# Kernel optimization log

Measured on AMD Instinct MI355X. Metric: run time of the kernel, lower is better.

The kernel has to match this reference:

```python
import jax, jax.numpy as jnp
import numpy as np

B, H, W, C_TOT = 8, 256, 256, 36
SIDX = slice(0, 3)    # special: Noll 1-3 -> 0-based 0..2
LIDX = slice(3, 6)    # low
MIDX = slice(6, 15)   # mid
HIDX = slice(15, 36)  # high


def _box3x3_sum(x):
    # x: [B, H, W]; 3x3 sliding-window sum with replicate (edge) padding.
    xp = jnp.pad(x, ((0, 0), (1, 1), (1, 1)), mode='edge')
    h, w = x.shape[1], x.shape[2]
    acc = jnp.zeros_like(x)
    for di in range(3):
        for dj in range(3):
            acc = acc + xp[:, di:di + h, dj:dj + w]
    return acc


def _group_core(z, bias, alpha, amax, eps, gss, p_sat):
    # z: [B, H, W, Cg]; all params shape [1]
    u = z + bias
    soft_abs = jnp.sqrt(u * u + eps)            # [B,H,W,Cg]
    s = _box3x3_sum(soft_abs.sum(axis=-1))      # [B,H,W] sum over channels and 3x3 window
    gain = gss / (1.0 + s / p_sat)              # [B,H,W]
    v = alpha * gain[..., None] * u
    return amax * jnp.tanh(v)


def setup_inputs() -> dict:
    key = jax.random.key(0)
    one = jnp.ones((1,), jnp.float32)
    inp = {
        'raw_coeffs': jax.random.normal(key, (B, H, W, C_TOT), dtype=jnp.float32),
        'special_bias': 0.0 * one, 'special_alpha': 1.0 * one,
        'special_amax': 1.0 * one, 'special_eps': 1e-6 * one,
        'low_bias': 0.0 * one, 'low_alpha': 1.0 * one, 'low_amax': 1.0 * one,
        'low_eps': 1e-6 * one, 'low_gss': 1.0 * one, 'low_p_sat': 1.0 * one,
        'mid_bias': 0.0 * one, 'mid_alpha': 1.0 * one, 'mid_amax': 1.0 * one,
        'mid_eps': 1e-6 * one, 'mid_gss': 1.0 * one, 'mid_p_sat': 1.0 * one,
        'high_bias': 0.0 * one, 'high_alpha': 1.0 * one, 'high_amax': 1.0 * one,
        'high_eps': 1e-6 * one, 'high_gss': 1.0 * one, 'high_p_sat': 1.0 * one,
    }
    return inp


def reference(raw_coeffs, special_bias, special_alpha, special_amax, special_eps,
              low_bias, low_alpha, low_amax, low_eps, low_gss, low_p_sat,
              mid_bias, mid_alpha, mid_amax, mid_eps, mid_gss, mid_p_sat,
              high_bias, high_alpha, high_amax, high_eps, high_gss, high_p_sat):
    # special group: plain affine + tanh (special_use_neighborhood=False)
    u_sp = raw_coeffs[..., SIDX] + special_bias
    out_sp = special_amax * jnp.tanh(special_alpha * u_sp)
    # local joint (3x3 coupled gain) groups
    out_lo = _group_core(raw_coeffs[..., LIDX], low_bias, low_alpha, low_amax, low_eps, low_gss, low_p_sat)
    out_mi = _group_core(raw_coeffs[..., MIDX], mid_bias, mid_alpha, mid_amax, mid_eps, mid_gss, mid_p_sat)
    out_hi = _group_core(raw_coeffs[..., HIDX], high_bias, high_alpha, high_amax, high_eps, high_gss, high_p_sat)
    return jnp.concatenate([out_sp, out_lo, out_mi, out_hi], axis=-1)
```

## Files before the change

kernel.cpp:

```cpp
#include <hip/hip_runtime.h>
#include <math.h>


static constexpr int IMG = 256;
static constexpr int NB = 8;
static constexpr int C = 36;
static constexpr int TS = 16;
static constexpr int HT = TS + 2;
static constexpr int ROWF4 = HT * 9;
static constexpr int NSTAGE4 = HT * HT * 9;
static constexpr int NOUT4 = TS * TS * 9;

__device__ __forceinline__ float fast_tanh(float x) {
    float e = __expf(2.0f * x);
    return 1.0f - __fdividef(2.0f, e + 1.0f);
}

__device__ __forceinline__ void group_sums(const float* __restrict__ v,
                                           float b_lo, float e_lo,
                                           float b_mi, float e_mi,
                                           float b_hi, float e_hi,
                                           float& tlo, float& tmi, float& thi) {
    float lo = 0.f, mi = 0.f, hi = 0.f;
    #pragma unroll
    for (int c = 3; c < 6; ++c)   { float u = v[c] + b_lo; lo += sqrtf(u * u + e_lo); }
    #pragma unroll
    for (int c = 6; c < 15; ++c)  { float u = v[c] + b_mi; mi += sqrtf(u * u + e_mi); }
    #pragma unroll
    for (int c = 15; c < 36; ++c) { float u = v[c] + b_hi; hi += sqrtf(u * u + e_hi); }
    tlo = lo; tmi = mi; thi = hi;
}

__global__ __launch_bounds__(256) void lgz_kernel(
    const float* __restrict__ in, float* __restrict__ out,
    const float* __restrict__ p_sp_bias, const float* __restrict__ p_sp_alpha,
    const float* __restrict__ p_sp_amax,
    const float* __restrict__ p_lo_bias, const float* __restrict__ p_lo_alpha,
    const float* __restrict__ p_lo_amax, const float* __restrict__ p_lo_eps,
    const float* __restrict__ p_lo_gss, const float* __restrict__ p_lo_psat,
    const float* __restrict__ p_mi_bias, const float* __restrict__ p_mi_alpha,
    const float* __restrict__ p_mi_amax, const float* __restrict__ p_mi_eps,
    const float* __restrict__ p_mi_gss, const float* __restrict__ p_mi_psat,
    const float* __restrict__ p_hi_bias, const float* __restrict__ p_hi_alpha,
    const float* __restrict__ p_hi_amax, const float* __restrict__ p_hi_eps,
    const float* __restrict__ p_hi_gss, const float* __restrict__ p_hi_psat)
{
    __shared__ __align__(16) float s_raw[HT * HT * C];
    __shared__ float s_sum[3][HT][HT + 1];

    const int tid = threadIdx.x;
    const int tx = tid & 15, ty = tid >> 4;
    const int bx0 = blockIdx.x * TS, by0 = blockIdx.y * TS;
    const int b = blockIdx.z;

    const float b_sp = p_sp_bias[0], a_sp = p_sp_alpha[0], m_sp = p_sp_amax[0];
    const float b_lo = p_lo_bias[0], a_lo = p_lo_alpha[0], m_lo = p_lo_amax[0];
    const float e_lo = p_lo_eps[0],  g_lo = p_lo_gss[0],  q_lo = p_lo_psat[0];
    const float b_mi = p_mi_bias[0], a_mi = p_mi_alpha[0], m_mi = p_mi_amax[0];
    const float e_mi = p_mi_eps[0],  g_mi = p_mi_gss[0],  q_mi = p_mi_psat[0];
    const float b_hi = p_hi_bias[0], a_hi = p_hi_alpha[0], m_hi = p_hi_amax[0];
    const float e_hi = p_hi_eps[0],  g_hi = p_hi_gss[0],  q_hi = p_hi_psat[0];

    const float* img = in + (size_t)b * IMG * IMG * C;
    float* outimg = out + (size_t)b * IMG * IMG * C;

    #pragma unroll
    for (int it = 0; it < (NSTAGE4 + 255) / 256; ++it) {
        int F4 = tid + it * 256;
        if (F4 < NSTAGE4) {
            int r = F4 / ROWF4;
            int rem = F4 - r * ROWF4;
            int px = rem / 9;
            int j = rem - px * 9;
            int gy = min(max(by0 + r - 1, 0), IMG - 1);
            int gx = min(max(bx0 + px - 1, 0), IMG - 1);
            float4 val = *reinterpret_cast<const float4*>(
                img + ((size_t)gy * IMG + gx) * C + j * 4);
            *reinterpret_cast<float4*>(s_raw + (r * HT + px) * C + j * 4) = val;
        }
    }
    __syncthreads();

    float v[C];
    {
        const float* src = s_raw + ((ty + 1) * HT + (tx + 1)) * C;
        #pragma unroll
        for (int j = 0; j < 9; ++j)
            reinterpret_cast<float4*>(v)[j] = reinterpret_cast<const float4*>(src)[j];
    }
    {
        float tlo, tmi, thi;
        group_sums(v, b_lo, e_lo, b_mi, e_mi, b_hi, e_hi, tlo, tmi, thi);
        s_sum[0][ty + 1][tx + 1] = tlo;
        s_sum[1][ty + 1][tx + 1] = tmi;
        s_sum[2][ty + 1][tx + 1] = thi;
    }
    if (tid < 68) {
        int hy, hx;
        if (tid < 18)      { hy = 0;            hx = tid; }
        else if (tid < 36) { hy = HT - 1;       hx = tid - 18; }
        else if (tid < 52) { hy = tid - 36 + 1; hx = 0; }
        else               { hy = tid - 52 + 1; hx = HT - 1; }
        float w[C];
        const float* src = s_raw + (hy * HT + hx) * C;
        #pragma unroll
        for (int j = 0; j < 9; ++j)
            reinterpret_cast<float4*>(w)[j] = reinterpret_cast<const float4*>(src)[j];
        float tlo, tmi, thi;
        group_sums(w, b_lo, e_lo, b_mi, e_mi, b_hi, e_hi, tlo, tmi, thi);
        s_sum[0][hy][hx] = tlo;
        s_sum[1][hy][hx] = tmi;
        s_sum[2][hy][hx] = thi;
    }
    __syncthreads();

    float slo = 0.f, smi = 0.f, shi = 0.f;
    #pragma unroll
    for (int di = 0; di < 3; ++di) {
        #pragma unroll
        for (int dj = 0; dj < 3; ++dj) {
            slo += s_sum[0][ty + di][tx + dj];
            smi += s_sum[1][ty + di][tx + dj];
            shi += s_sum[2][ty + di][tx + dj];
        }
    }
    const float glo = a_lo * __fdividef(g_lo, 1.0f + __fdividef(slo, q_lo));
    const float gmi = a_mi * __fdividef(g_mi, 1.0f + __fdividef(smi, q_mi));
    const float ghi = a_hi * __fdividef(g_hi, 1.0f + __fdividef(shi, q_hi));

    #pragma unroll
    for (int c = 0; c < 3; ++c)   v[c] = m_sp * fast_tanh(a_sp * (v[c] + b_sp));
    #pragma unroll
    for (int c = 3; c < 6; ++c)   v[c] = m_lo * fast_tanh(glo * (v[c] + b_lo));
    #pragma unroll
    for (int c = 6; c < 15; ++c)  v[c] = m_mi * fast_tanh(gmi * (v[c] + b_mi));
    #pragma unroll
    for (int c = 15; c < 36; ++c) v[c] = m_hi * fast_tanh(ghi * (v[c] + b_hi));

    {
        float* dst = s_raw + ((ty + 1) * HT + (tx + 1)) * C;
        #pragma unroll
        for (int j = 0; j < 9; ++j)
            reinterpret_cast<float4*>(dst)[j] = reinterpret_cast<const float4*>(v)[j];
    }
    __syncthreads();

    #pragma unroll
    for (int it = 0; it < NOUT4 / 256; ++it) {
        int F4 = tid + it * 256;
        int p = F4 / 9;
        int j = F4 - p * 9;
        int r = p >> 4, cc = p & 15;
        float4 val = *reinterpret_cast<const float4*>(
            s_raw + ((r + 1) * HT + (cc + 1)) * C + 4 * j);
        *reinterpret_cast<float4*>(
            outimg + ((size_t)(by0 + r) * IMG + (bx0 + cc)) * C + 4 * j) = val;
    }
}

extern "C" void kernel_launch(void* const* d_in, const int* in_sizes, int n_in,
                              void* d_out, int out_size, void* d_ws, size_t ws_size,
                              hipStream_t stream) {
    const float* raw = (const float*)d_in[0];
    dim3 grid(IMG / TS, IMG / TS, NB);
    dim3 block(256);
    lgz_kernel<<<grid, block, 0, stream>>>(
        raw, (float*)d_out,
        (const float*)d_in[1], (const float*)d_in[2], (const float*)d_in[3],
        (const float*)d_in[5], (const float*)d_in[6], (const float*)d_in[7],
        (const float*)d_in[8], (const float*)d_in[9], (const float*)d_in[10],
        (const float*)d_in[11], (const float*)d_in[12], (const float*)d_in[13],
        (const float*)d_in[14], (const float*)d_in[15], (const float*)d_in[16],
        (const float*)d_in[17], (const float*)d_in[18], (const float*)d_in[19],
        (const float*)d_in[20], (const float*)d_in[21], (const float*)d_in[22]);
}
```

Baseline: 47.24 us.

## Keep raw tile in registers, reduce group sums via shared atomics

The kernel no longer stages the 18x18x36 raw tile in shared memory. Each thread holds a fixed float4 channel slot for 12 halo-tile pixels in registers and adds its partial per-group soft-abs sums into a small shared float4-per-pixel array with shared atomics. Gains are computed once per interior pixel into shared memory, and the outputs are written straight from registers to global memory. This also folds the constants of tanh into the gain. The aim is to cut shared-memory footprint and traffic and raise occupancy, at the cost of shared atomics, higher register pressure and 4 idle lanes per block.

```diff
diff --git a/kernel.cpp b/kernel.cpp
--- a/kernel.cpp
+++ b/kernel.cpp
@@ -7,29 +7,10 @@
 static constexpr int C = 36;
 static constexpr int TS = 16;
 static constexpr int HT = TS + 2;
-static constexpr int ROWF4 = HT * 9;
-static constexpr int NSTAGE4 = HT * HT * 9;
-static constexpr int NOUT4 = TS * TS * 9;
-
-__device__ __forceinline__ float fast_tanh(float x) {
-    float e = __expf(2.0f * x);
-    return 1.0f - __fdividef(2.0f, e + 1.0f);
-}
-
-__device__ __forceinline__ void group_sums(const float* __restrict__ v,
-                                           float b_lo, float e_lo,
-                                           float b_mi, float e_mi,
-                                           float b_hi, float e_hi,
-                                           float& tlo, float& tmi, float& thi) {
-    float lo = 0.f, mi = 0.f, hi = 0.f;
-    #pragma unroll
-    for (int c = 3; c < 6; ++c)   { float u = v[c] + b_lo; lo += sqrtf(u * u + e_lo); }
-    #pragma unroll
-    for (int c = 6; c < 15; ++c)  { float u = v[c] + b_mi; mi += sqrtf(u * u + e_mi); }
-    #pragma unroll
-    for (int c = 15; c < 36; ++c) { float u = v[c] + b_hi; hi += sqrtf(u * u + e_hi); }
-    tlo = lo; tmi = mi; thi = hi;
-}
+static constexpr int NPIX = HT * HT;
+static constexpr int ACT = 252;
+static constexpr int PSTEP = 28;
+static constexpr int NSWEEP = 12;
 
 __global__ __launch_bounds__(256) void lgz_kernel(
     const float* __restrict__ in, float* __restrict__ out,
@@ -45,13 +26,14 @@
     const float* __restrict__ p_hi_amax, const float* __restrict__ p_hi_eps,
     const float* __restrict__ p_hi_gss, const float* __restrict__ p_hi_psat)
 {
-    __shared__ __align__(16) float s_raw[HT * HT * C];
-    __shared__ float s_sum[3][HT][HT + 1];
+    __shared__ float4 s_sum4[NPIX];
+    __shared__ float4 s_gain4[NPIX];
+    float* ss = reinterpret_cast<float*>(s_sum4);
 
     const int tid = threadIdx.x;
-    const int tx = tid & 15, ty = tid >> 4;
     const int bx0 = blockIdx.x * TS, by0 = blockIdx.y * TS;
-    const int b = blockIdx.z;
+    const float* img = in + (size_t)blockIdx.z * IMG * IMG * C;
+    float* oimg = out + (size_t)blockIdx.z * IMG * IMG * C;
 
     const float b_sp = p_sp_bias[0], a_sp = p_sp_alpha[0], m_sp = p_sp_amax[0];
     const float b_lo = p_lo_bias[0], a_lo = p_lo_alpha[0], m_lo = p_lo_amax[0];
@@ -61,100 +43,120 @@
     const float b_hi = p_hi_bias[0], a_hi = p_hi_alpha[0], m_hi = p_hi_amax[0];
     const float e_hi = p_hi_eps[0],  g_hi = p_hi_gss[0],  q_hi = p_hi_psat[0];
 
-    const float* img = in + (size_t)b * IMG * IMG * C;
-    float* outimg = out + (size_t)b * IMG * IMG * C;
+    const float Clo = 2.0f * a_lo * g_lo, inv_qlo = __fdividef(1.0f, q_lo);
+    const float Cmi = 2.0f * a_mi * g_mi, inv_qmi = __fdividef(1.0f, q_mi);
+    const float Chi = 2.0f * a_hi * g_hi, inv_qhi = __fdividef(1.0f, q_hi);
+    const float G_sp = 2.0f * a_sp;
 
+    const float4 z4 = make_float4(0.f, 0.f, 0.f, 0.f);
+    for (int i = tid; i < NPIX; i += 256) s_sum4[i] = z4;
+
+    const bool active = tid < ACT;
+    const int j = tid % 9;
+    const int p0 = tid / 9;
+    const int c0 = 4 * j;
+    float biasK[4], epsK[4], amaxK[4], amax2K[4];
     #pragma unroll
-    for (int it = 0; it < (NSTAGE4 + 255) / 256; ++it) {
-        int F4 = tid + it * 256;
-        if (F4 < NSTAGE4) {
-            int r = F4 / ROWF4;
-            int rem = F4 - r * ROWF4;
-            int px = rem / 9;
-            int j = rem - px * 9;
-            int gy = min(max(by0 + r - 1, 0), IMG - 1);
-            int gx = min(max(bx0 + px - 1, 0), IMG - 1);
-            float4 val = *reinterpret_cast<const float4*>(
-                img + ((size_t)gy * IMG + gx) * C + j * 4);
-            *reinterpret_cast<float4*>(s_raw + (r * HT + px) * C + j * 4) = val;
+    for (int k = 0; k < 4; ++k) {
+        const int c = c0 + k;
+        biasK[k]  = c < 3 ? b_sp : (c < 6 ? b_lo : (c < 15 ? b_mi : b_hi));
+        epsK[k]   = c < 6 ? e_lo : (c < 15 ? e_mi : e_hi);
+        const float mm = c < 3 ? m_sp : (c < 6 ? m_lo : (c < 15 ? m_mi : m_hi));
+        amaxK[k] = mm; amax2K[k] = 2.0f * mm;
+    }
+    #define GRP(c) ((c) < 3 ? 3 : ((c) < 6 ? 0 : ((c) < 15 ? 1 : 2)))
+    const int gA = GRP(c0), gB = GRP(c0 + 3);
+    const int ks = 1 + (GRP(c0 + 1) == gA) + (GRP(c0 + 2) == gA) + (GRP(c0 + 3) == gA);
+    #undef GRP
+
+    float4 x[NSWEEP];
+    int voff[NSWEEP];
+    unsigned pmask = 0;
+    {
+        int p = p0;
+        #pragma unroll
+        for (int s = 0; s < NSWEEP; ++s, p += PSTEP) {
+            const bool val = active && p < NPIX;
+            const int r = p / HT, px = p - r * HT;
+            const int gy = min(max(by0 + r - 1, 0), IMG - 1);
+            const int gx = min(max(bx0 + px - 1, 0), IMG - 1);
+            const int vo = ((gy << 8) + gx) * (C * 4) + j * 16;
+            voff[s] = vo;
+            const bool inter = (unsigned)(r - 1) < (unsigned)TS &&
+                               (unsigned)(px - 1) < (unsigned)TS;
+            if (val && inter) pmask |= (1u << s);
+            x[s] = val ? *reinterpret_cast<const float4*>(
+                             reinterpret_cast<const char*>(img) + vo)
+                       : z4;
         }
     }
     __syncthreads();
 
-    float v[C];
     {
-        const float* src = s_raw + ((ty + 1) * HT + (tx + 1)) * C;
+        int p = p0;
         #pragma unroll
-        for (int j = 0; j < 9; ++j)
-            reinterpret_cast<float4*>(v)[j] = reinterpret_cast<const float4*>(src)[j];
-    }
-    {
-        float tlo, tmi, thi;
-        group_sums(v, b_lo, e_lo, b_mi, e_mi, b_hi, e_hi, tlo, tmi, thi);
-        s_sum[0][ty + 1][tx + 1] = tlo;
-        s_sum[1][ty + 1][tx + 1] = tmi;
-        s_sum[2][ty + 1][tx + 1] = thi;
-    }
-    if (tid < 68) {
-        int hy, hx;
-        if (tid < 18)      { hy = 0;            hx = tid; }
-        else if (tid < 36) { hy = HT - 1;       hx = tid - 18; }
-        else if (tid < 52) { hy = tid - 36 + 1; hx = 0; }
-        else               { hy = tid - 52 + 1; hx = HT - 1; }
-        float w[C];
-        const float* src = s_raw + (hy * HT + hx) * C;
-        #pragma unroll
-        for (int j = 0; j < 9; ++j)
-            reinterpret_cast<float4*>(w)[j] = reinterpret_cast<const float4*>(src)[j];
-        float tlo, tmi, thi;
-        group_sums(w, b_lo, e_lo, b_mi, e_mi, b_hi, e_hi, tlo, tmi, thi);
-        s_sum[0][hy][hx] = tlo;
-        s_sum[1][hy][hx] = tmi;
-        s_sum[2][hy][hx] = thi;
+        for (int s = 0; s < NSWEEP; ++s, p += PSTEP) {
+            const bool val = active && p < NPIX;
+            if (val) {
+                const float xs[4] = {x[s].x, x[s].y, x[s].z, x[s].w};
+                float t[4];
+                #pragma unroll
+                for (int k = 0; k < 4; ++k) {
+                    const float u = xs[k] + biasK[k];
+                    t[k] = sqrtf(fmaf(u, u, epsK[k]));
+                }
+                const float tot = (t[0] + t[1]) + (t[2] + t[3]);
+                float segA = t[0];
+                if (ks > 1) segA += t[1];
+                if (ks > 2) segA += t[2];
+                if (ks > 3) segA += t[3];
+                const float segB = tot - segA;
+                if (gA != 3) atomicAdd(&ss[p * 4 + gA], segA);
+                if (ks < 4) atomicAdd(&ss[p * 4 + gB], segB);
+            }
+        }
     }
     __syncthreads();
 
-    float slo = 0.f, smi = 0.f, shi = 0.f;
-    #pragma unroll
-    for (int di = 0; di < 3; ++di) {
+    {
+        const int r = (tid >> 4) + 1, px = (tid & 15) + 1;
+        float slo = 0.f, smi = 0.f, shi = 0.f;
         #pragma unroll
-        for (int dj = 0; dj < 3; ++dj) {
-            slo += s_sum[0][ty + di][tx + dj];
-            smi += s_sum[1][ty + di][tx + dj];
-            shi += s_sum[2][ty + di][tx + dj];
+        for (int dr = -1; dr <= 1; ++dr) {
+            #pragma unroll
+            for (int dc = -1; dc <= 1; ++dc) {
+                const float4 v = s_sum4[(r + dr) * HT + (px + dc)];
+                slo += v.x; smi += v.y; shi += v.z;
+            }
         }
-    }
-    const float glo = a_lo * __fdividef(g_lo, 1.0f + __fdividef(slo, q_lo));
-    const float gmi = a_mi * __fdividef(g_mi, 1.0f + __fdividef(smi, q_mi));
-    const float ghi = a_hi * __fdividef(g_hi, 1.0f + __fdividef(shi, q_hi));
-
-    #pragma unroll
-    for (int c = 0; c < 3; ++c)   v[c] = m_sp * fast_tanh(a_sp * (v[c] + b_sp));
-    #pragma unroll
-    for (int c = 3; c < 6; ++c)   v[c] = m_lo * fast_tanh(glo * (v[c] + b_lo));
-    #pragma unroll
-    for (int c = 6; c < 15; ++c)  v[c] = m_mi * fast_tanh(gmi * (v[c] + b_mi));
-    #pragma unroll
-    for (int c = 15; c < 36; ++c) v[c] = m_hi * fast_tanh(ghi * (v[c] + b_hi));
-
-    {
-        float* dst = s_raw + ((ty + 1) * HT + (tx + 1)) * C;
-        #pragma unroll
-        for (int j = 0; j < 9; ++j)
-            reinterpret_cast<float4*>(dst)[j] = reinterpret_cast<const float4*>(v)[j];
+        const float Gl = __fdividef(Clo, fmaf(slo, inv_qlo, 1.0f));
+        const float Gm = __fdividef(Cmi, fmaf(smi, inv_qmi, 1.0f));
+        const float Gh = __fdividef(Chi, fmaf(shi, inv_qhi, 1.0f));
+        s_gain4[r * HT + px] = make_float4(Gl, Gm, Gh, 0.f);
     }
     __syncthreads();
 
-    #pragma unroll
-    for (int it = 0; it < NOUT4 / 256; ++it) {
-        int F4 = tid + it * 256;
-        int p = F4 / 9;
-        int j = F4 - p * 9;
-        int r = p >> 4, cc = p & 15;
-        float4 val = *reinterpret_cast<const float4*>(
-            s_raw + ((r + 1) * HT + (cc + 1)) * C + 4 * j);
-        *reinterpret_cast<float4*>(
-            outimg + ((size_t)(by0 + r) * IMG + (bx0 + cc)) * C + 4 * j) = val;
+    {
+        int p = p0;
+        #pragma unroll
+        for (int s = 0; s < NSWEEP; ++s, p += PSTEP) {
+            if ((pmask >> s) & 1u) {
+                const float4 g = s_gain4[p];
+                const float GA = gA == 0 ? g.x : (gA == 1 ? g.y : (gA == 2 ? g.z : G_sp));
+                const float GB = gB == 0 ? g.x : (gB == 1 ? g.y : g.z);
+                const float xs[4] = {x[s].x, x[s].y, x[s].z, x[s].w};
+                float o[4];
+                #pragma unroll
+                for (int k = 0; k < 4; ++k) {
+                    const float G = (k < ks) ? GA : GB;
+                    const float u = xs[k] + biasK[k];
+                    const float e = __expf(G * u);
+                    o[k] = amaxK[k] - __fdividef(amax2K[k], e + 1.0f);
+                }
+                *reinterpret_cast<float4*>(reinterpret_cast<char*>(oimg) + voff[s]) =
+                    make_float4(o[0], o[1], o[2], o[3]);
+            }
+        }
     }
 }
 
```

New measurement: 75.55 us. +59.9%, slower.
